# Kernel tuning notes

Measured on AMD Instinct MI355X. Metric: run time of the kernel, lower is better.

Reference implementation:

```python
import jax, jax.numpy as jnp
import numpy as np

HID, H, HD, K, L = 512, 8, 64, 64, 767  # hidden, heads, head_dim, clip, coord length
B, S = 2, L + 1  # add_cls pads one token


def _rel_indices(coords, k):
    # torch.cdist p=2: pairwise euclidean distances [B, L, L]
    diff = coords[:, :, None, :] - coords[:, None, :, :]
    dist = jnp.sqrt(jnp.sum(diff * diff, axis=-1))
    # rank along rows / columns via double argsort
    t1 = jnp.argsort(jnp.argsort(dist, axis=-1), axis=-1)
    t2 = jnp.argsort(jnp.argsort(dist, axis=-2), axis=-2)
    nm = jnp.triu(t1, k=1) + jnp.tril(t2, k=1)
    nm = jnp.clip(nm, 0, k)
    # add_cls: prepend a zero column then a zero row -> [B, L+1, L+1]
    nm = jnp.pad(nm, ((0, 0), (1, 0), (1, 0)))
    return nm.astype(jnp.int32)


def setup_inputs() -> dict:
    key = jax.random.key(0)
    ks = jax.random.split(key, 16)
    sc = 0.05
    return {
        "query": jax.random.normal(ks[0], (B, S, HID), jnp.float32),
        "key": jax.random.normal(ks[1], (B, S, HID), jnp.float32),
        "value": jax.random.normal(ks[2], (B, S, HID), jnp.float32),
        "coords": jax.random.normal(ks[3], (B, L, 2), jnp.float32),
        "Wq": jax.random.normal(ks[4], (H, HID, HD), jnp.float32) * sc,
        "bq": jax.random.normal(ks[5], (H, HD), jnp.float32) * sc,
        "Wk": jax.random.normal(ks[6], (H, HID, HD), jnp.float32) * sc,
        "bk": jax.random.normal(ks[7], (H, HD), jnp.float32) * sc,
        "Wv": jax.random.normal(ks[8], (H, HID, HD), jnp.float32) * sc,
        "bv": jax.random.normal(ks[9], (H, HD), jnp.float32) * sc,
        "pe_k": jax.random.normal(ks[10], (K + 1, HD), jnp.float32) * sc,
        "pe_v": jax.random.normal(ks[11], (K + 1, HD), jnp.float32) * sc,
        "fc_W": jax.random.normal(ks[12], (HID, HID), jnp.float32) * sc,
        "fc_b": jax.random.normal(ks[13], (HID,), jnp.float32) * sc,
    }


def reference(query, key, value, coords, Wq, bq, Wk, bk, Wv, bv, pe_k, pe_v, fc_W, fc_b):
    idx = _rel_indices(coords, K)                 # [B, S, S] int
    k_bias = pe_k[idx]                            # [B, S, S, HD]
    v_bias = pe_v[idx]                            # [B, S, S, HD]

    # per-head projections, heads stacked on axis n
    q = jnp.einsum('bsh,nhd->bnsd', query, Wq) + bq[None, :, None, :]
    k = jnp.einsum('bsh,nhd->bnsd', key, Wk) + bk[None, :, None, :]
    v = jnp.einsum('bsh,nhd->bnsd', value, Wv) + bv[None, :, None, :]

    attn1 = jnp.einsum('bnqd,bnkd->bnqk', q, k)
    attn2 = jnp.einsum('bnqd,bqkd->bnqk', q, k_bias)  # per-query relative key bias
    att = jax.nn.softmax((attn1 + attn2) / (HD ** 0.5), axis=-1)

    out1 = jnp.einsum('bnqk,bnkd->bnqd', att, v)
    out2 = jnp.einsum('bnqk,bqkd->bnqd', att, v_bias)  # relative value bias
    heads = (out1 + out2).transpose(0, 2, 1, 3).reshape(B, S, H * HD)  # concat heads
    return heads @ fc_W.T + fc_b
```

## Files before the change

kernel.cpp:

```cpp
#include <hip/hip_runtime.h>
#include <math.h>

#define HIDD 512
#define NH 8
#define HD 64
#define KCLIP 64
#define LCO 767
#define BB 2
#define SS 768

#define TQ 32
#define KT 64
#define NT (SS / KT)
#define KS 4
#define TPB (NT / KS)
#define NROW (BB * NH * SS)
#define QPAD 68

__global__ __launch_bounds__(256) void idx_fill_kernel(int* __restrict__ idx)
{
    size_t gid = (size_t)blockIdx.x * 256 + threadIdx.x;
    size_t base = gid * 4;
    int rem = (int)(base % (size_t)(SS * SS));
    int r = rem / SS, c0 = rem % SS;
    int4 v;
    int* vv = (int*)&v;
#pragma unroll
    for (int u = 0; u < 4; ++u) {
        int c = c0 + u;
        vv[u] = (r == 0 || c == 0 || r == c) ? 0 : KCLIP;
    }
    *(int4*)(idx + base) = v;
}

__global__ __launch_bounds__(256) void rel_idx_kernel(
    const float* __restrict__ coords, int* __restrict__ idx)
{
    __shared__ float cx[LCO], cy[LCO];
    __shared__ unsigned long long dk[LCO];
    __shared__ unsigned long long lst[LCO];
    __shared__ int hist[256];
    __shared__ int cum[256];
    __shared__ int nsel;
    __shared__ int thrB;

    const int blk = blockIdx.x;
    const int b = blk / LCO;
    const int i = blk % LCO;
    const int t = threadIdx.x;
    const float* cb = coords + (size_t)b * LCO * 2;

    hist[t] = 0;
    if (t == 0) nsel = 0;
    for (int j = t; j < LCO; j += 256) {
        float2 c2 = *(const float2*)(cb + 2 * j);
        cx[j] = c2.x; cy[j] = c2.y;
    }
    __syncthreads();
    const float xi = cx[i], yi = cy[i];
    for (int j = t; j < LCO; j += 256) {
        float dx = xi - cx[j];
        float dy = yi - cy[j];
        float d2 = __fadd_rn(__fmul_rn(dx, dx), __fmul_rn(dy, dy));
        float d = sqrtf(d2);
        dk[j] = ((unsigned long long)__float_as_uint(d) << 32) | (unsigned)j;
        int bkt = (int)(d * 32.0f);
        bkt = bkt > 255 ? 255 : bkt;
        atomicAdd(&hist[bkt], 1);
    }
    __syncthreads();

    cum[t] = hist[t];
    __syncthreads();
    for (int off = 1; off < 256; off <<= 1) {
        int add = (t >= off) ? cum[t - off] : 0;
        __syncthreads();
        cum[t] += add;
        __syncthreads();
    }
    if (cum[t] >= KCLIP && (t == 0 || cum[t - 1] < KCLIP)) thrB = t;
    __syncthreads();
    const int B = thrB;

    const int lane = t & 63;
#pragma unroll
    for (int u = 0; u < 3; ++u) {
        int j = t + u * 256;
        bool sel = false;
        unsigned long long key = 0;
        if (j < LCO) {
            key = dk[j];
            float d = __uint_as_float((unsigned)(key >> 32));
            int bkt = (int)(d * 32.0f);
            bkt = bkt > 255 ? 255 : bkt;
            sel = (bkt <= B);
        }
        unsigned long long m = __ballot(sel);
        int base;
        if (lane == 0) base = atomicAdd(&nsel, __popcll(m));
        base = __shfl(base, 0);
        if (sel) {
            int pfx = __popcll(m & ((1ull << lane) - 1));
            lst[base + pfx] = key;
        }
    }
    __syncthreads();
    const int C = nsel;

    int* ib = idx + (size_t)b * SS * SS;
    for (int c = t; c < C; c += 256) {
        unsigned long long myk = lst[c];
        int cnt = 0;
        for (int c2 = 0; c2 < C; ++c2) cnt += (lst[c2] < myk);
        int j = (int)(myk & 0xffffffffu);
        if (cnt < KCLIP && j > i) {
            ib[(size_t)(i + 1) * SS + (j + 1)] = cnt;
            ib[(size_t)(j + 1) * SS + (i + 1)] = cnt;
        }
    }
}

__global__ __launch_bounds__(256) void proj_kernel(
    const float* __restrict__ qin, const float* __restrict__ kin, const float* __restrict__ vin,
    const float* __restrict__ Wq, const float* __restrict__ Wk, const float* __restrict__ Wv,
    const float* __restrict__ bq, const float* __restrict__ bk, const float* __restrict__ bv,
    float* __restrict__ qo, float* __restrict__ kTo, float* __restrict__ vo)
{
    const int z = blockIdx.z;
    const float* A = (z == 0) ? qin : (z == 1) ? kin : vin;
    const float* W = (z == 0) ? Wq : (z == 1) ? Wk : Wv;
    const float* bias = (z == 0) ? bq : (z == 1) ? bk : bv;
    const int h = blockIdx.y;
    const int m0 = blockIdx.x * 64;

    __shared__ float As[32][68];
    __shared__ float Bs[32][64];

    const int t = threadIdx.x;
    const int tx = t & 15, ty = t >> 4;
    const float* Wh = W + (size_t)h * HIDD * HD;

    float acc[4][4] = {};
    for (int k0 = 0; k0 < HIDD; k0 += 32) {
#pragma unroll
        for (int u = 0; u < 2; ++u) {
            int i = t + u * 256;
            int row = i >> 3, kc = (i & 7) * 4;
            float4 a4 = *(const float4*)(A + (size_t)(m0 + row) * HIDD + k0 + kc);
            As[kc + 0][row] = a4.x; As[kc + 1][row] = a4.y;
            As[kc + 2][row] = a4.z; As[kc + 3][row] = a4.w;
            int kr = i >> 4, n4 = (i & 15) * 4;
            *(float4*)(&Bs[kr][n4]) = *(const float4*)(Wh + (size_t)(k0 + kr) * HD + n4);
        }
        __syncthreads();
#pragma unroll
        for (int kk = 0; kk < 32; ++kk) {
            float4 a4 = *(const float4*)(&As[kk][ty * 4]);
            float4 b4 = *(const float4*)(&Bs[kk][tx * 4]);
            float a_[4] = {a4.x, a4.y, a4.z, a4.w};
            float b_[4] = {b4.x, b4.y, b4.z, b4.w};
#pragma unroll
            for (int r = 0; r < 4; ++r)
#pragma unroll
                for (int c = 0; c < 4; ++c) acc[r][c] += a_[r] * b_[c];
        }
        __syncthreads();
    }
#pragma unroll
    for (int r = 0; r < 4; ++r) {
        int m = m0 + ty * 4 + r;
        int bIdx = m / SS, s = m % SS;
#pragma unroll
        for (int c = 0; c < 4; ++c) {
            int d = tx * 4 + c;
            float val = acc[r][c] + bias[h * HD + d];
            if (z == 1) {
                kTo[((size_t)(bIdx * NH + h) * HD + d) * SS + s] = val;
            } else {
                float* O = (z == 0) ? qo : vo;
                O[((size_t)(bIdx * NH + h) * SS + s) * HD + d] = val;
            }
        }
    }
}

__global__ __launch_bounds__(256) void qpk_kernel(
    const float* __restrict__ q, const float* __restrict__ pe_k, float* __restrict__ qpkg)
{
    __shared__ float qs[64][68];
    __shared__ float pk[65][68];
    const int t = threadIdx.x;
    const int q0 = blockIdx.x * 64;
    const int bn = blockIdx.y;
    const float* qbase = q + ((size_t)bn * SS + q0) * HD;
    for (int i = t; i < 64 * 16; i += 256) {
        int row = i >> 4, d4 = (i & 15) * 4;
        *(float4*)(&qs[row][d4]) = *(const float4*)(qbase + (size_t)row * HD + d4);
    }
    for (int i = t; i < 65 * 16; i += 256) {
        int c = i >> 4, d4 = (i & 15) * 4;
        *(float4*)(&pk[c][d4]) = *(const float4*)(pe_k + (size_t)c * HD + d4);
    }
    __syncthreads();
    const int r0 = t >> 2, cg = t & 3;
    float* orow = qpkg + ((size_t)bn * SS + q0 + r0) * QPAD;
    for (int c = cg; c <= KCLIP; c += 4) {
        float acc = 0.f;
#pragma unroll
        for (int d4 = 0; d4 < HD; d4 += 4) {
            float4 qv = *(const float4*)(&qs[r0][d4]);
            float4 pv = *(const float4*)(&pk[c][d4]);
            acc += qv.x * pv.x + qv.y * pv.y + qv.z * pv.z + qv.w * pv.w;
        }
        orow[c] = acc;
    }
}

__global__ __launch_bounds__(256) void attn_part_kernel(
    const float* __restrict__ q, const float* __restrict__ kT,
    const float* __restrict__ vb, const int* __restrict__ idx,
    const float* __restrict__ qpkg,
    float* __restrict__ o1p, float* __restrict__ pspart, float* __restrict__ wbpart)
{
    __shared__ float qsT[HD][TQ];
    __shared__ float kv[KT][HD];
    __shared__ float attQ[TQ][68];
    __shared__ float qpkS[TQ][68];
    __shared__ float wbuf[TQ][KCLIP];

    const int t = threadIdx.x;
    const int bn = blockIdx.y;
    const int b = bn >> 3;
    const int q0 = blockIdx.x * TQ;
    const int ks = blockIdx.z;

    const int qh = t >> 4;
    const int kg = t & 15;

    const float* qbase = q + ((size_t)bn * SS + q0) * HD;
    for (int i = t; i < TQ * 16; i += 256) {
        int r = i >> 4, dx = (i & 15) * 4;
        float4 v4 = *(const float4*)(qbase + (size_t)r * HD + dx);
        qsT[dx + 0][r] = v4.x; qsT[dx + 1][r] = v4.y;
        qsT[dx + 2][r] = v4.z; qsT[dx + 3][r] = v4.w;
    }
    for (int i = t; i < TQ * 17; i += 256) {
        int r = i / 17, c4 = (i % 17) * 4;
        *(float4*)(&qpkS[r][c4]) = *(const float4*)(qpkg + ((size_t)bn * SS + q0 + r) * QPAD + c4);
    }
    for (int i = t; i < TQ * KCLIP; i += 256) ((float*)wbuf)[i] = 0.f;
    __syncthreads();

    const float* kTbn = kT + (size_t)bn * HD * SS;
    const float* vbn = vb + (size_t)bn * SS * HD;
    const int* ib = idx + (size_t)b * SS * SS;

    float out1[2][4] = {};
    float psum[2] = {0.f, 0.f};

    for (int t0 = 0; t0 < TPB; ++t0) {
        const int k0 = (ks * TPB + t0) * KT;
        for (int i = t; i < KT * 16; i += 256) {
            int d = i >> 4, c4 = (i & 15) * 4;
            *(float4*)(&kv[d][c4]) = *(const float4*)(kTbn + (size_t)d * SS + k0 + c4);
        }
        __syncthreads();

        float acc[2][4] = {};
#pragma unroll 16
        for (int d = 0; d < HD; ++d) {
            float q0v = qsT[d][2 * qh];
            float q1v = qsT[d][2 * qh + 1];
            float4 k4 = *(const float4*)(&kv[d][4 * kg]);
            acc[0][0] += q0v * k4.x; acc[0][1] += q0v * k4.y;
            acc[0][2] += q0v * k4.z; acc[0][3] += q0v * k4.w;
            acc[1][0] += q1v * k4.x; acc[1][1] += q1v * k4.y;
            acc[1][2] += q1v * k4.z; acc[1][3] += q1v * k4.w;
        }
#pragma unroll
        for (int e = 0; e < 2; ++e) {
            int qq = 2 * qh + e;
            int4 iv = *(const int4*)(ib + (size_t)(q0 + qq) * SS + k0 + 4 * kg);
            float p0 = expf((acc[e][0] + qpkS[qq][iv.x]) * 0.125f);
            float p1 = expf((acc[e][1] + qpkS[qq][iv.y]) * 0.125f);
            float p2 = expf((acc[e][2] + qpkS[qq][iv.z]) * 0.125f);
            float p3 = expf((acc[e][3] + qpkS[qq][iv.w]) * 0.125f);
            float4 pv4; pv4.x = p0; pv4.y = p1; pv4.z = p2; pv4.w = p3;
            *(float4*)(&attQ[qq][4 * kg]) = pv4;
            if (iv.x < KCLIP) atomicAdd(&wbuf[qq][iv.x], p0);
            if (iv.y < KCLIP) atomicAdd(&wbuf[qq][iv.y], p1);
            if (iv.z < KCLIP) atomicAdd(&wbuf[qq][iv.z], p2);
            if (iv.w < KCLIP) atomicAdd(&wbuf[qq][iv.w], p3);
            psum[e] += p0 + p1 + p2 + p3;
        }
        __syncthreads();

        for (int i = t; i < KT * 16; i += 256) {
            int k = i >> 4, d4 = (i & 15) * 4;
            *(float4*)(&kv[k][d4]) = *(const float4*)(vbn + (size_t)(k0 + k) * HD + d4);
        }
        __syncthreads();

#pragma unroll 16
        for (int k = 0; k < KT; ++k) {
            float a0 = attQ[2 * qh][k];
            float a1 = attQ[2 * qh + 1][k];
            float4 v4 = *(const float4*)(&kv[k][4 * kg]);
            out1[0][0] += a0 * v4.x; out1[0][1] += a0 * v4.y;
            out1[0][2] += a0 * v4.z; out1[0][3] += a0 * v4.w;
            out1[1][0] += a1 * v4.x; out1[1][1] += a1 * v4.y;
            out1[1][2] += a1 * v4.z; out1[1][3] += a1 * v4.w;
        }
        __syncthreads();
    }

#pragma unroll
    for (int off = 8; off; off >>= 1) {
        psum[0] += __shfl_xor(psum[0], off);
        psum[1] += __shfl_xor(psum[1], off);
    }
    const size_t rbase = (size_t)ks * NROW + (size_t)bn * SS + q0;
    if (kg == 0) {
        pspart[rbase + 2 * qh] = psum[0];
        pspart[rbase + 2 * qh + 1] = psum[1];
    }
#pragma unroll
    for (int e = 0; e < 2; ++e) {
        int qq = 2 * qh + e;
        *(float4*)(o1p + (rbase + qq) * HD + 4 * kg) = *(float4*)(out1[e]);
    }
    for (int i = t; i < TQ * KCLIP / 4; i += 256) {
        int r = i >> 4, c4 = (i & 15) * 4;
        *(float4*)(wbpart + (rbase + r) * KCLIP + c4) = *(const float4*)(&wbuf[r][c4]);
    }
}

__global__ __launch_bounds__(256) void attn_combine_kernel(
    const float* __restrict__ o1p, const float* __restrict__ pspart,
    const float* __restrict__ wbpart, const float* __restrict__ pe_v,
    float* __restrict__ heads)
{
    __shared__ float wl[4][66];
    const int t = threadIdx.x;
    const int rt = t >> 6, d = t & 63;
    const int row = blockIdx.x * 4 + rt;
    const int bn = row / SS, qq = row % SS;
    const int b = bn >> 3, n = bn & 7;

    float w = 0.f, rsum = 0.f, o = 0.f;
#pragma unroll
    for (int ks = 0; ks < KS; ++ks) {
        w += wbpart[((size_t)ks * NROW + row) * KCLIP + d];
        rsum += pspart[(size_t)ks * NROW + row];
        o += o1p[((size_t)ks * NROW + row) * HD + d];
    }
    wl[rt][d] = w;
    __syncthreads();

    const float pv64 = pe_v[KCLIP * HD + d];
    float acc = o;
#pragma unroll 8
    for (int c = 0; c < KCLIP; ++c)
        acc += wl[rt][c] * (pe_v[c * HD + d] - pv64);
    heads[((size_t)b * SS + qq) * HIDD + n * HD + d] = acc / rsum + pv64;
}

__global__ __launch_bounds__(256) void fc_kernel(
    const float* __restrict__ heads, const float* __restrict__ fcW,
    const float* __restrict__ fcb, float* __restrict__ out)
{
    const int m0 = blockIdx.x * 32;
    const int n0 = blockIdx.y * 64;

    __shared__ float As[32][36];
    __shared__ float Bs[32][64];

    const int t = threadIdx.x;
    const int ty = t >> 4;
    const int tx = t & 15;

    float acc[2][4] = {};
    for (int k0 = 0; k0 < HIDD; k0 += 32) {
        {
            int row = t >> 3, kc = (t & 7) * 4;
            float4 a4 = *(const float4*)(heads + (size_t)(m0 + row) * HIDD + k0 + kc);
            As[kc + 0][row] = a4.x; As[kc + 1][row] = a4.y;
            As[kc + 2][row] = a4.z; As[kc + 3][row] = a4.w;
        }
#pragma unroll
        for (int u = 0; u < 2; ++u) {
            int i = t + u * 256;
            int nl = i >> 3, kl = (i & 7) * 4;
            float4 bw = *(const float4*)(fcW + (size_t)(n0 + nl) * HIDD + k0 + kl);
            Bs[kl + 0][nl] = bw.x; Bs[kl + 1][nl] = bw.y;
            Bs[kl + 2][nl] = bw.z; Bs[kl + 3][nl] = bw.w;
        }
        __syncthreads();
#pragma unroll
        for (int kk = 0; kk < 32; ++kk) {
            float a0 = As[kk][2 * ty];
            float a1 = As[kk][2 * ty + 1];
            float4 b4 = *(const float4*)(&Bs[kk][4 * tx]);
            acc[0][0] += a0 * b4.x; acc[0][1] += a0 * b4.y;
            acc[0][2] += a0 * b4.z; acc[0][3] += a0 * b4.w;
            acc[1][0] += a1 * b4.x; acc[1][1] += a1 * b4.y;
            acc[1][2] += a1 * b4.z; acc[1][3] += a1 * b4.w;
        }
        __syncthreads();
    }
    float4 bb = *(const float4*)(fcb + n0 + 4 * tx);
#pragma unroll
    for (int e = 0; e < 2; ++e) {
        float4 r4;
        r4.x = acc[e][0] + bb.x; r4.y = acc[e][1] + bb.y;
        r4.z = acc[e][2] + bb.z; r4.w = acc[e][3] + bb.w;
        *(float4*)(out + (size_t)(m0 + 2 * ty + e) * HIDD + n0 + 4 * tx) = r4;
    }
}

extern "C" void kernel_launch(void* const* d_in, const int* in_sizes, int n_in,
                              void* d_out, int out_size, void* d_ws, size_t ws_size,
                              hipStream_t stream)
{
    (void)in_sizes; (void)n_in; (void)out_size; (void)ws_size;
    const float* query  = (const float*)d_in[0];
    const float* key_   = (const float*)d_in[1];
    const float* value  = (const float*)d_in[2];
    const float* coords = (const float*)d_in[3];
    const float* Wq = (const float*)d_in[4];
    const float* bq = (const float*)d_in[5];
    const float* Wk = (const float*)d_in[6];
    const float* bk = (const float*)d_in[7];
    const float* Wv = (const float*)d_in[8];
    const float* bv = (const float*)d_in[9];
    const float* pe_k = (const float*)d_in[10];
    const float* pe_v = (const float*)d_in[11];
    const float* fcW  = (const float*)d_in[12];
    const float* fcb  = (const float*)d_in[13];
    float* out = (float*)d_out;

    char* ws = (char*)d_ws;
    size_t off = 0;
    auto alloc = [&](size_t bytes) -> void* {
        void* p = ws + off;
        off += (bytes + 255) & ~(size_t)255;
        return p;
    };
    int*   idx    = (int*)  alloc((size_t)BB * SS * SS * sizeof(int));
    float* qb     = (float*)alloc((size_t)BB * NH * SS * HD * sizeof(float));
    float* kTb    = (float*)alloc((size_t)BB * NH * HD * SS * sizeof(float));
    float* vb     = (float*)alloc((size_t)BB * NH * SS * HD * sizeof(float));
    float* headb  = (float*)alloc((size_t)BB * SS * HIDD * sizeof(float));
    float* qpkg   = (float*)alloc((size_t)NROW * QPAD * sizeof(float));
    float* o1p    = (float*)alloc((size_t)KS * NROW * HD * sizeof(float));
    float* pspart = (float*)alloc((size_t)KS * NROW * sizeof(float));
    float* wbpart = (float*)alloc((size_t)KS * NROW * KCLIP * sizeof(float));

    idx_fill_kernel<<<(BB * SS * SS) / (256 * 4), 256, 0, stream>>>(idx);

    rel_idx_kernel<<<BB * LCO, 256, 0, stream>>>(coords, idx);

    proj_kernel<<<dim3((BB * SS) / 64, NH, 3), 256, 0, stream>>>(
        query, key_, value, Wq, Wk, Wv, bq, bk, bv, qb, kTb, vb);

    qpk_kernel<<<dim3(SS / 64, BB * NH), 256, 0, stream>>>(qb, pe_k, qpkg);

    attn_part_kernel<<<dim3(SS / TQ, BB * NH, KS), 256, 0, stream>>>(
        qb, kTb, vb, idx, qpkg, o1p, pspart, wbpart);

    attn_combine_kernel<<<NROW / 4, 256, 0, stream>>>(o1p, pspart, wbpart, pe_v, headb);

    fc_kernel<<<dim3((BB * SS) / 32, HIDD / 64), 256, 0, stream>>>(headb, fcW, fcb, out);
}
```

Measured before the change: 247.2 us.

## Remap attention thread tiling and store probabilities transposed in shared memory

The QK^T stage now gives each thread 4 queries by 2 keys instead of 2 queries by 4 keys, so a warp of 32 lanes spans 64 keys of a single query group. Probabilities are written key-major into a padded attP buffer, which lets the PV stage read two queries with one float2 load instead of two scalar loads. expf is replaced by the faster __expf intrinsic, and the psum reduction moves to a 32-lane shuffle. The intent is fewer shared-memory bank conflicts and a cheaper exponential, at the cost of slightly reduced precision and a different pattern of atomic contention on wbuf.

```diff
diff --git a/kernel.cpp b/kernel.cpp
--- a/kernel.cpp
+++ b/kernel.cpp
@@ -224,8 +224,8 @@
 {
     __shared__ float qsT[HD][TQ];
     __shared__ float kv[KT][HD];
-    __shared__ float attQ[TQ][68];
-    __shared__ float qpkS[TQ][68];
+    __shared__ float attP[KT][36];
+    __shared__ float qpkS[TQ][QPAD];
     __shared__ float wbuf[TQ][KCLIP];
 
     const int t = threadIdx.x;
@@ -234,8 +234,10 @@
     const int q0 = blockIdx.x * TQ;
     const int ks = blockIdx.z;
 
-    const int qh = t >> 4;
-    const int kg = t & 15;
+    const int qg = t >> 5;
+    const int kg = t & 31;
+    const int qg2 = t >> 4;
+    const int dg = t & 15;
 
     const float* qbase = q + ((size_t)bn * SS + q0) * HD;
     for (int i = t; i < TQ * 16; i += 256) {
@@ -256,7 +258,7 @@
     const int* ib = idx + (size_t)b * SS * SS;
 
     float out1[2][4] = {};
-    float psum[2] = {0.f, 0.f};
+    float psum[4] = {0.f, 0.f, 0.f, 0.f};
 
     for (int t0 = 0; t0 < TPB; ++t0) {
         const int k0 = (ks * TPB + t0) * KT;
@@ -266,32 +268,35 @@
         }
         __syncthreads();
 
-        float acc[2][4] = {};
+        float acc[4][2] = {};
 #pragma unroll 16
         for (int d = 0; d < HD; ++d) {
-            float q0v = qsT[d][2 * qh];
-            float q1v = qsT[d][2 * qh + 1];
-            float4 k4 = *(const float4*)(&kv[d][4 * kg]);
-            acc[0][0] += q0v * k4.x; acc[0][1] += q0v * k4.y;
-            acc[0][2] += q0v * k4.z; acc[0][3] += q0v * k4.w;
-            acc[1][0] += q1v * k4.x; acc[1][1] += q1v * k4.y;
-            acc[1][2] += q1v * k4.z; acc[1][3] += q1v * k4.w;
-        }
-#pragma unroll
-        for (int e = 0; e < 2; ++e) {
-            int qq = 2 * qh + e;
-            int4 iv = *(const int4*)(ib + (size_t)(q0 + qq) * SS + k0 + 4 * kg);
-            float p0 = expf((acc[e][0] + qpkS[qq][iv.x]) * 0.125f);
-            float p1 = expf((acc[e][1] + qpkS[qq][iv.y]) * 0.125f);
-            float p2 = expf((acc[e][2] + qpkS[qq][iv.z]) * 0.125f);
-            float p3 = expf((acc[e][3] + qpkS[qq][iv.w]) * 0.125f);
-            float4 pv4; pv4.x = p0; pv4.y = p1; pv4.z = p2; pv4.w = p3;
-            *(float4*)(&attQ[qq][4 * kg]) = pv4;
+            float4 qv = *(const float4*)(&qsT[d][4 * qg]);
+            float2 k2 = *(const float2*)(&kv[d][2 * kg]);
+            float q_[4] = {qv.x, qv.y, qv.z, qv.w};
+#pragma unroll
+            for (int r = 0; r < 4; ++r) {
+                acc[r][0] += q_[r] * k2.x;
+                acc[r][1] += q_[r] * k2.y;
+            }
+        }
+        float pr0[4], pr1[4];
+#pragma unroll
+        for (int r = 0; r < 4; ++r) {
+            int qq = 4 * qg + r;
+            int2 iv = *(const int2*)(ib + (size_t)(q0 + qq) * SS + k0 + 2 * kg);
+            float p0 = __expf((acc[r][0] + qpkS[qq][iv.x]) * 0.125f);
+            float p1 = __expf((acc[r][1] + qpkS[qq][iv.y]) * 0.125f);
             if (iv.x < KCLIP) atomicAdd(&wbuf[qq][iv.x], p0);
             if (iv.y < KCLIP) atomicAdd(&wbuf[qq][iv.y], p1);
-            if (iv.z < KCLIP) atomicAdd(&wbuf[qq][iv.z], p2);
-            if (iv.w < KCLIP) atomicAdd(&wbuf[qq][iv.w], p3);
-            psum[e] += p0 + p1 + p2 + p3;
+            psum[r] += p0 + p1;
+            pr0[r] = p0; pr1[r] = p1;
+        }
+        {
+            float4 w0; w0.x = pr0[0]; w0.y = pr0[1]; w0.z = pr0[2]; w0.w = pr0[3];
+            float4 w1; w1.x = pr1[0]; w1.y = pr1[1]; w1.z = pr1[2]; w1.w = pr1[3];
+            *(float4*)(&attP[2 * kg + 0][4 * qg]) = w0;
+            *(float4*)(&attP[2 * kg + 1][4 * qg]) = w1;
         }
         __syncthreads();
 
@@ -302,32 +307,31 @@
         __syncthreads();
 
 #pragma unroll 16
-        for (int k = 0; k < KT; ++k) {
-            float a0 = attQ[2 * qh][k];
-            float a1 = attQ[2 * qh + 1][k];
-            float4 v4 = *(const float4*)(&kv[k][4 * kg]);
-            out1[0][0] += a0 * v4.x; out1[0][1] += a0 * v4.y;
-            out1[0][2] += a0 * v4.z; out1[0][3] += a0 * v4.w;
-            out1[1][0] += a1 * v4.x; out1[1][1] += a1 * v4.y;
-            out1[1][2] += a1 * v4.z; out1[1][3] += a1 * v4.w;
-        }
-        __syncthreads();
-    }
-
-#pragma unroll
-    for (int off = 8; off; off >>= 1) {
-        psum[0] += __shfl_xor(psum[0], off);
-        psum[1] += __shfl_xor(psum[1], off);
+        for (int kk = 0; kk < KT; ++kk) {
+            float2 a2 = *(const float2*)(&attP[kk][2 * qg2]);
+            float4 v4 = *(const float4*)(&kv[kk][4 * dg]);
+            out1[0][0] += a2.x * v4.x; out1[0][1] += a2.x * v4.y;
+            out1[0][2] += a2.x * v4.z; out1[0][3] += a2.x * v4.w;
+            out1[1][0] += a2.y * v4.x; out1[1][1] += a2.y * v4.y;
+            out1[1][2] += a2.y * v4.z; out1[1][3] += a2.y * v4.w;
+        }
+        __syncthreads();
+    }
+
+#pragma unroll
+    for (int off = 16; off; off >>= 1) {
+#pragma unroll
+        for (int r = 0; r < 4; ++r) psum[r] += __shfl_xor(psum[r], off);
     }
     const size_t rbase = (size_t)ks * NROW + (size_t)bn * SS + q0;
     if (kg == 0) {
-        pspart[rbase + 2 * qh] = psum[0];
-        pspart[rbase + 2 * qh + 1] = psum[1];
+#pragma unroll
+        for (int r = 0; r < 4; ++r) pspart[rbase + 4 * qg + r] = psum[r];
     }
 #pragma unroll
     for (int e = 0; e < 2; ++e) {
-        int qq = 2 * qh + e;
-        *(float4*)(o1p + (rbase + qq) * HD + 4 * kg) = *(float4*)(out1[e]);
+        int qq = 2 * qg2 + e;
+        *(float4*)(o1p + (rbase + qq) * HD + 4 * dg) = *(float4*)(out1[e]);
     }
     for (int i = t; i < TQ * KCLIP / 4; i += 256) {
         int r = i >> 4, c4 = (i & 15) * 4;
```

Result: slower. 268.5 us (+8.6%).
